# Kernel optimization log

Hardware: AMD Instinct MI355X
Metric: run time of the kernel (lower is better)

## Reference

```python
import jax, jax.numpy as jnp
import numpy as np

S = 7
B = 2
CLS = 20
N = CLS + B * 5  # 30
LAMBDA_COORD = 5.0
LAMBDA_NOOBJ = 0.5
BATCH = 16384


def setup_inputs() -> dict:
    key = jax.random.key(0)
    k1, k2, k3 = jax.random.split(key, 3)
    pred = jax.random.uniform(k1, (BATCH, S, S, N), dtype=jnp.float32)
    target = jax.random.uniform(k2, (BATCH, S, S, N), dtype=jnp.float32)
    # conf channel (index 4) must be exactly 0 or 1 -- it drives the obj/noobj masks
    obj = (jax.random.uniform(k3, (BATCH, S, S)) < 0.15).astype(jnp.float32)
    target = target.at[..., 4].set(obj)
    return {"pred": pred, "target": target}


def _iou(b1, b2):
    # b1: [M, B, 4] xyxy, b2: [M, 4] xyxy -> [M, B]
    lt = jnp.maximum(b1[..., :2], b2[:, None, :2])
    rb = jnp.minimum(b1[..., 2:], b2[:, None, 2:])
    wh = jnp.clip(rb - lt, 0.0)
    inter = wh[..., 0] * wh[..., 1]
    area1 = (b1[..., 2] - b1[..., 0]) * (b1[..., 3] - b1[..., 1])
    area2 = ((b2[:, 2] - b2[:, 0]) * (b2[:, 3] - b2[:, 1]))[:, None]
    union = area1 + area2 - inter
    return jnp.where(union > 0, inter / union, 0.0)


def reference(pred, target):
    batch = pred.shape[0]
    p = pred.reshape(-1, N)   # [M, 30], M = batch*S*S
    t = target.reshape(-1, N)
    obj = (t[:, 4] == 1).astype(pred.dtype)    # positive-cell mask
    noobj = (t[:, 4] == 0).astype(pred.dtype)  # negative-cell mask

    # faithful to source: conf_loc = arange(B)*B + 4 -> [4, 6]
    conf_loc = jnp.arange(B) * B + 4
    noobj_conf_loss = jnp.sum(noobj[:, None] * (p[:, conf_loc] - t[:, conf_loc]) ** 2)

    pb = p[:, : B * 5].reshape(-1, B, 5)  # [M, B, 5] (x, y, w, h, conf)
    tb = t[:, :5]                         # [M, 5] first target box per cell

    # xywh -> xyxy
    pb_xyxy = jnp.concatenate([pb[..., :2] - pb[..., 2:4] / 2,
                               pb[..., :2] + pb[..., 2:4] / 2], axis=-1)
    tb_xyxy = jnp.concatenate([tb[:, :2] - tb[:, 2:4] / 2,
                               tb[:, :2] + tb[:, 2:4] / 2], axis=-1)

    iou = _iou(pb_xyxy, tb_xyxy)                         # [M, B]
    j = jnp.argmax(iou, axis=1)                          # responsible box index
    max_iou = jax.lax.stop_gradient(jnp.max(iou, axis=1))
    resp = jnp.take_along_axis(pb, j[:, None, None], axis=1)[:, 0]  # [M, 5]

    xy_loss = jnp.sum((resp[:, :2] - tb[:, :2]) ** 2, axis=-1)
    wh_loss = jnp.sum((jnp.sqrt(jnp.clip(resp[:, 2:4], 0.0))
                       - jnp.sqrt(jnp.clip(tb[:, 2:4], 0.0))) ** 2, axis=-1)
    coord_loss = jnp.sum(obj * (xy_loss + wh_loss))

    obj_conf_loss = jnp.sum(obj * (resp[:, 4] - max_iou) ** 2)
    class_loss = jnp.sum(obj[:, None] * (p[:, B * 5:] - t[:, B * 5:]) ** 2)

    total = (LAMBDA_COORD * coord_loss + obj_conf_loss
             + LAMBDA_NOOBJ * noobj_conf_loss + class_loss) / batch
    return total
```

## Files before the change

kernel.cpp:

```cpp
#include <hip/hip_runtime.h>


#define TPB 256
#define NPER 30
#define R_TOTAL (16384 * 7 * 7)
#define NBLOCKS (R_TOTAL / TPB)

__global__ __launch_bounds__(TPB, 4) void yolo_loss_kernel(
    const float* __restrict__ pred, const float* __restrict__ target,
    float* __restrict__ out)
{
    __shared__ float red[TPB / 64];

    const int tid = threadIdx.x;
    const size_t cell = (size_t)blockIdx.x * TPB + tid;

    float p[NPER], t[NPER];
    {
        const float2* gp = (const float2*)(pred + cell * NPER);
        const float2* gt = (const float2*)(target + cell * NPER);
        #pragma unroll
        for (int i = 0; i < NPER / 2; i++) {
            float2 v = gp[i];
            p[2 * i] = v.x; p[2 * i + 1] = v.y;
        }
        #pragma unroll
        for (int i = 0; i < NPER / 2; i++) {
            float2 v = gt[i];
            t[2 * i] = v.x; t[2 * i + 1] = v.y;
        }
    }

    float sum = 0.0f;
    const float t4 = t[4];
    if (t4 == 0.0f) {
        float d4 = p[4] - t[4];
        float d6 = p[6] - t[6];
        sum = 0.5f * (d4 * d4 + d6 * d6);
    } else if (t4 == 1.0f) {
        float tx1 = t[0] - t[2] * 0.5f, ty1 = t[1] - t[3] * 0.5f;
        float tx2 = t[0] + t[2] * 0.5f, ty2 = t[1] + t[3] * 0.5f;
        float area2 = (tx2 - tx1) * (ty2 - ty1);

        float ax1 = p[0] - p[2] * 0.5f, ay1 = p[1] - p[3] * 0.5f;
        float ax2 = p[0] + p[2] * 0.5f, ay2 = p[1] + p[3] * 0.5f;
        float w0 = fmaxf(fminf(ax2, tx2) - fmaxf(ax1, tx1), 0.0f);
        float h0 = fmaxf(fminf(ay2, ty2) - fmaxf(ay1, ty1), 0.0f);
        float inter0 = w0 * h0;
        float uni0 = (ax2 - ax1) * (ay2 - ay1) + area2 - inter0;
        float iou0 = (uni0 > 0.0f) ? (inter0 / uni0) : 0.0f;

        float bx1 = p[5] - p[7] * 0.5f, by1 = p[6] - p[8] * 0.5f;
        float bx2 = p[5] + p[7] * 0.5f, by2 = p[6] + p[8] * 0.5f;
        float w1 = fmaxf(fminf(bx2, tx2) - fmaxf(bx1, tx1), 0.0f);
        float h1 = fmaxf(fminf(by2, ty2) - fmaxf(by1, ty1), 0.0f);
        float inter1 = w1 * h1;
        float uni1 = (bx2 - bx1) * (by2 - by1) + area2 - inter1;
        float iou1 = (uni1 > 0.0f) ? (inter1 / uni1) : 0.0f;

        bool j1 = (iou1 > iou0);
        float max_iou = fmaxf(iou0, iou1);
        float r0 = j1 ? p[5] : p[0];
        float r1 = j1 ? p[6] : p[1];
        float r2 = j1 ? p[7] : p[2];
        float r3 = j1 ? p[8] : p[3];
        float r4 = j1 ? p[9] : p[4];

        float dx = r0 - t[0];
        float dy = r1 - t[1];
        float sw = sqrtf(fmaxf(r2, 0.0f)) - sqrtf(fmaxf(t[2], 0.0f));
        float sh = sqrtf(fmaxf(r3, 0.0f)) - sqrtf(fmaxf(t[3], 0.0f));
        float coord = dx * dx + dy * dy + sw * sw + sh * sh;
        float dc = r4 - max_iou;

        float cls = 0.0f;
        #pragma unroll
        for (int k = 10; k < NPER; k++) {
            float d = p[k] - t[k];
            cls += d * d;
        }
        sum = 5.0f * coord + dc * dc + cls;
    }

    #pragma unroll
    for (int off = 32; off > 0; off >>= 1)
        sum += __shfl_down(sum, off, 64);
    if ((tid & 63) == 0) red[tid >> 6] = sum;
    __syncthreads();
    if (tid == 0) {
        float s = red[0] + red[1] + red[2] + red[3];
        atomicAdd(out, s * (1.0f / 16384.0f));
    }
}

extern "C" void kernel_launch(void* const* d_in, const int* in_sizes, int n_in,
                              void* d_out, int out_size, void* d_ws, size_t ws_size,
                              hipStream_t stream) {
    const float* pred = (const float*)d_in[0];
    const float* target = (const float*)d_in[1];
    float* out = (float*)d_out;
    hipMemsetAsync(out, 0, sizeof(float), stream);
    yolo_loss_kernel<<<NBLOCKS, TPB, 0, stream>>>(pred, target, out);
}
```

Measured before the change: 211.4 us.

## Coalesce global loads via block-wide float2 striding and LDS transpose

Replaces the per-thread strided 120-byte row loads with block-cooperative, fully coalesced float2 loads. Each element is scattered into padded shared-memory arrays holding only the box and target fields each cell needs. Class-loss squared differences are accumulated into per-cell shared slots with LDS atomics during the load. The aim is better global-memory coalescing, paid for with extra LDS traffic, shared atomics, index arithmetic and a reduced-occupancy shared footprint.

Result: slower. 235.0 us (+11.2%).

```diff
diff --git a/kernel.cpp b/kernel.cpp
--- a/kernel.cpp
+++ b/kernel.cpp
@@ -5,31 +5,59 @@
 #define NPER 30
 #define R_TOTAL (16384 * 7 * 7)
 #define NBLOCKS (R_TOTAL / TPB)
+#define PB_STRIDE 11
+#define TB_STRIDE 7
 
 __global__ __launch_bounds__(TPB, 4) void yolo_loss_kernel(
     const float* __restrict__ pred, const float* __restrict__ target,
     float* __restrict__ out)
 {
+    __shared__ float pb[TPB * PB_STRIDE];
+    __shared__ float tb[TPB * TB_STRIDE];
+    __shared__ float cls[TPB];
     __shared__ float red[TPB / 64];
 
     const int tid = threadIdx.x;
-    const size_t cell = (size_t)blockIdx.x * TPB + tid;
+    cls[tid] = 0.0f;
+    __syncthreads();
 
-    float p[NPER], t[NPER];
-    {
-        const float2* gp = (const float2*)(pred + cell * NPER);
-        const float2* gt = (const float2*)(target + cell * NPER);
-        #pragma unroll
-        for (int i = 0; i < NPER / 2; i++) {
-            float2 v = gp[i];
-            p[2 * i] = v.x; p[2 * i + 1] = v.y;
-        }
-        #pragma unroll
-        for (int i = 0; i < NPER / 2; i++) {
-            float2 v = gt[i];
-            t[2 * i] = v.x; t[2 * i + 1] = v.y;
+    const size_t base = (size_t)blockIdx.x * (TPB * NPER);
+    const float2* gp = (const float2*)(pred + base);
+    const float2* gt = (const float2*)(target + base);
+
+    #pragma unroll
+    for (int k = 0; k < (TPB * NPER) / (2 * TPB); k++) {
+        int F = tid + k * TPB;
+        float2 vp = gp[F];
+        float2 vt = gt[F];
+        unsigned f0 = 2u * (unsigned)F;
+        unsigned c0 = (f0 * 34953u) >> 20;
+        int s0 = (int)(f0 - c0 * 30u);
+        int s1 = s0 + 1;
+        unsigned c1 = c0;
+        if (s1 == 30) { s1 = 0; c1 = c0 + 1; }
+
+        if (s0 < 10) pb[c0 * PB_STRIDE + s0] = vp.x;
+        if (s1 < 10) pb[c1 * PB_STRIDE + s1] = vp.y;
+        if (s0 < 7)  tb[c0 * TB_STRIDE + s0] = vt.x;
+        if (s1 < 7)  tb[c1 * TB_STRIDE + s1] = vt.y;
+
+        float d0 = vp.x - vt.x;
+        float d1 = vp.y - vt.y;
+        if (c1 == c0) {
+            if (s1 >= 10) {
+                float e = d1 * d1;
+                if (s0 >= 10) e += d0 * d0;
+                atomicAdd(&cls[c0], e);
+            }
+        } else {
+            atomicAdd(&cls[c0], d0 * d0);
         }
     }
+    __syncthreads();
+
+    const float* p = &pb[tid * PB_STRIDE];
+    const float* t = &tb[tid * TB_STRIDE];
 
     float sum = 0.0f;
     const float t4 = t[4];
@@ -73,13 +101,7 @@
         float coord = dx * dx + dy * dy + sw * sw + sh * sh;
         float dc = r4 - max_iou;
 
-        float cls = 0.0f;
-        #pragma unroll
-        for (int k = 10; k < NPER; k++) {
-            float d = p[k] - t[k];
-            cls += d * d;
-        }
-        sum = 5.0f * coord + dc * dc + cls;
+        sum = 5.0f * coord + dc * dc + cls[tid];
     }
 
     #pragma unroll
```

## Coalesce tile loads with float4 streaming and gate per-cell work via shared mask

Applied to the files above, without the earlier changes.

Each block now handles 512 cells as a contiguous tile. It first stages each cell's confidence flag in shared memory, then streams both inputs with fully coalesced float4 loads. Each element finds its cell and channel with a multiply-shift divide and adds to class or no-object sums depending on the cached flag. Object cells then reload their first ten predicted values and first four target values to compute the IoU and coordinate terms. This replaces the strided per-thread float2 loads, which were poorly coalesced, at the cost of an extra scattered gather of t[4], a second partial read for object cells, and more index arithmetic per element.

Result: slower. 249.1 us (+17.8%).

```diff
diff --git a/kernel.cpp b/kernel.cpp
--- a/kernel.cpp
+++ b/kernel.cpp
@@ -3,84 +3,113 @@
 
 #define TPB 256
 #define NPER 30
+#define CPB 512
+#define TILE_FLOATS (CPB * NPER)
 #define R_TOTAL (16384 * 7 * 7)
-#define NBLOCKS (R_TOTAL / TPB)
+#define NBLOCKS (R_TOTAL / CPB)
 
 __global__ __launch_bounds__(TPB, 4) void yolo_loss_kernel(
     const float* __restrict__ pred, const float* __restrict__ target,
     float* __restrict__ out)
 {
+    __shared__ float t4s[CPB];
     __shared__ float red[TPB / 64];
 
     const int tid = threadIdx.x;
-    const size_t cell = (size_t)blockIdx.x * TPB + tid;
+    const size_t tbase = (size_t)blockIdx.x * TILE_FLOATS;
+    const float* gp = pred + tbase;
+    const float* gt = target + tbase;
 
-    float p[NPER], t[NPER];
-    {
-        const float2* gp = (const float2*)(pred + cell * NPER);
-        const float2* gt = (const float2*)(target + cell * NPER);
+    t4s[tid]       = gt[(size_t)tid * NPER + 4];
+    t4s[tid + TPB] = gt[(size_t)(tid + TPB) * NPER + 4];
+    __syncthreads();
+
+    float acc_cls = 0.0f;
+    float acc_no  = 0.0f;
+
+    const float4* gp4 = (const float4*)gp;
+    const float4* gt4 = (const float4*)gt;
+    #pragma unroll
+    for (int k = 0; k < TILE_FLOATS / (4 * TPB); k++) {
+        int F = tid + k * TPB;
+        float4 vp = gp4[F];
+        float4 vt = gt4[F];
+        unsigned f0 = 4u * (unsigned)F;
+        unsigned c0 = (f0 * 34953u) >> 20;
+        int s0 = (int)(f0 - c0 * 30u);
+        float gA = t4s[c0];
+        float gB = (s0 == 28) ? t4s[c0 + 1] : gA;
+
+        float pe[4] = {vp.x, vp.y, vp.z, vp.w};
+        float te[4] = {vt.x, vt.y, vt.z, vt.w};
         #pragma unroll
-        for (int i = 0; i < NPER / 2; i++) {
-            float2 v = gp[i];
-            p[2 * i] = v.x; p[2 * i + 1] = v.y;
-        }
-        #pragma unroll
-        for (int i = 0; i < NPER / 2; i++) {
-            float2 v = gt[i];
-            t[2 * i] = v.x; t[2 * i + 1] = v.y;
+        for (int i = 0; i < 4; i++) {
+            int s = s0 + i;
+            float g = gA;
+            if (s >= 30) { s -= 30; g = gB; }
+            float d = pe[i] - te[i];
+            float q = d * d;
+            bool is_cls = (s >= 10);
+            bool is_no  = (s == 4) | (s == 6);
+            acc_cls += (is_cls && (g == 1.0f)) ? q : 0.0f;
+            acc_no  += (is_no  && (g == 0.0f)) ? q : 0.0f;
         }
     }
 
-    float sum = 0.0f;
-    const float t4 = t[4];
-    if (t4 == 0.0f) {
-        float d4 = p[4] - t[4];
-        float d6 = p[6] - t[6];
-        sum = 0.5f * (d4 * d4 + d6 * d6);
-    } else if (t4 == 1.0f) {
-        float tx1 = t[0] - t[2] * 0.5f, ty1 = t[1] - t[3] * 0.5f;
-        float tx2 = t[0] + t[2] * 0.5f, ty2 = t[1] + t[3] * 0.5f;
-        float area2 = (tx2 - tx1) * (ty2 - ty1);
+    float acc_obj = 0.0f;
+    #pragma unroll
+    for (int cc = 0; cc < CPB / TPB; cc++) {
+        int c = tid + cc * TPB;
+        if (t4s[c] == 1.0f) {
+            const float* p = gp + (size_t)c * NPER;
+            const float* t = gt + (size_t)c * NPER;
+            float2 p01 = *(const float2*)(p + 0);
+            float2 p23 = *(const float2*)(p + 2);
+            float2 p45 = *(const float2*)(p + 4);
+            float2 p67 = *(const float2*)(p + 6);
+            float2 p89 = *(const float2*)(p + 8);
+            float2 t01 = *(const float2*)(t + 0);
+            float2 t23 = *(const float2*)(t + 2);
 
-        float ax1 = p[0] - p[2] * 0.5f, ay1 = p[1] - p[3] * 0.5f;
-        float ax2 = p[0] + p[2] * 0.5f, ay2 = p[1] + p[3] * 0.5f;
-        float w0 = fmaxf(fminf(ax2, tx2) - fmaxf(ax1, tx1), 0.0f);
-        float h0 = fmaxf(fminf(ay2, ty2) - fmaxf(ay1, ty1), 0.0f);
-        float inter0 = w0 * h0;
-        float uni0 = (ax2 - ax1) * (ay2 - ay1) + area2 - inter0;
-        float iou0 = (uni0 > 0.0f) ? (inter0 / uni0) : 0.0f;
+            float tx1 = t01.x - t23.x * 0.5f, ty1 = t01.y - t23.y * 0.5f;
+            float tx2 = t01.x + t23.x * 0.5f, ty2 = t01.y + t23.y * 0.5f;
+            float area2 = (tx2 - tx1) * (ty2 - ty1);
 
-        float bx1 = p[5] - p[7] * 0.5f, by1 = p[6] - p[8] * 0.5f;
-        float bx2 = p[5] + p[7] * 0.5f, by2 = p[6] + p[8] * 0.5f;
-        float w1 = fmaxf(fminf(bx2, tx2) - fmaxf(bx1, tx1), 0.0f);
-        float h1 = fmaxf(fminf(by2, ty2) - fmaxf(by1, ty1), 0.0f);
-        float inter1 = w1 * h1;
-        float uni1 = (bx2 - bx1) * (by2 - by1) + area2 - inter1;
-        float iou1 = (uni1 > 0.0f) ? (inter1 / uni1) : 0.0f;
+            float ax1 = p01.x - p23.x * 0.5f, ay1 = p01.y - p23.y * 0.5f;
+            float ax2 = p01.x + p23.x * 0.5f, ay2 = p01.y + p23.y * 0.5f;
+            float w0 = fmaxf(fminf(ax2, tx2) - fmaxf(ax1, tx1), 0.0f);
+            float h0 = fmaxf(fminf(ay2, ty2) - fmaxf(ay1, ty1), 0.0f);
+            float inter0 = w0 * h0;
+            float uni0 = (ax2 - ax1) * (ay2 - ay1) + area2 - inter0;
+            float iou0 = (uni0 > 0.0f) ? (inter0 / uni0) : 0.0f;
 
-        bool j1 = (iou1 > iou0);
-        float max_iou = fmaxf(iou0, iou1);
-        float r0 = j1 ? p[5] : p[0];
-        float r1 = j1 ? p[6] : p[1];
-        float r2 = j1 ? p[7] : p[2];
-        float r3 = j1 ? p[8] : p[3];
-        float r4 = j1 ? p[9] : p[4];
+            float bx1 = p45.y - p67.y * 0.5f, by1 = p67.x - p89.x * 0.5f;
+            float bx2 = p45.y + p67.y * 0.5f, by2 = p67.x + p89.x * 0.5f;
+            float w1 = fmaxf(fminf(bx2, tx2) - fmaxf(bx1, tx1), 0.0f);
+            float h1 = fmaxf(fminf(by2, ty2) - fmaxf(by1, ty1), 0.0f);
+            float inter1 = w1 * h1;
+            float uni1 = (bx2 - bx1) * (by2 - by1) + area2 - inter1;
+            float iou1 = (uni1 > 0.0f) ? (inter1 / uni1) : 0.0f;
 
-        float dx = r0 - t[0];
-        float dy = r1 - t[1];
-        float sw = sqrtf(fmaxf(r2, 0.0f)) - sqrtf(fmaxf(t[2], 0.0f));
-        float sh = sqrtf(fmaxf(r3, 0.0f)) - sqrtf(fmaxf(t[3], 0.0f));
-        float coord = dx * dx + dy * dy + sw * sw + sh * sh;
-        float dc = r4 - max_iou;
+            bool j1 = (iou1 > iou0);
+            float max_iou = fmaxf(iou0, iou1);
+            float r0 = j1 ? p45.y : p01.x;
+            float r1 = j1 ? p67.x : p01.y;
+            float r2 = j1 ? p67.y : p23.x;
+            float r3 = j1 ? p89.x : p23.y;
+            float r4 = j1 ? p89.y : p45.x;
 
-        float cls = 0.0f;
-        #pragma unroll
-        for (int k = 10; k < NPER; k++) {
-            float d = p[k] - t[k];
-            cls += d * d;
+            float dx = r0 - t01.x;
+            float dy = r1 - t01.y;
+            float sw = sqrtf(fmaxf(r2, 0.0f)) - sqrtf(fmaxf(t23.x, 0.0f));
+            float sh = sqrtf(fmaxf(r3, 0.0f)) - sqrtf(fmaxf(t23.y, 0.0f));
+            float coord = dx * dx + dy * dy + sw * sw + sh * sh;
+            float dc = r4 - max_iou;
+            acc_obj += 5.0f * coord + dc * dc;
         }
-        sum = 5.0f * coord + dc * dc + cls;
     }
+
+    float sum = acc_cls + 0.5f * acc_no + acc_obj;
 
     #pragma unroll
     for (int off = 32; off > 0; off >>= 1)
```
